# Kernel tuning notes

Hardware: AMD Instinct MI355X
Metric: run time of the kernel (lower is better)

## Reference

```python
import jax, jax.numpy as jnp
import numpy as np

K = 16  # top-k patches kept (module default)

def setup_inputs() -> dict:
    key = jax.random.key(0)
    ks = jax.random.split(key, 5)
    N, D, A, H = 100000, 1024, 128, 256
    x = jax.random.normal(ks[0], (N, D), dtype=jnp.float32)
    Wa1 = jax.random.normal(ks[1], (D, A), dtype=jnp.float32) * (1.0 / np.sqrt(D))
    ba1 = jnp.zeros((A,), dtype=jnp.float32)
    Wa2 = jax.random.normal(ks[2], (A, 1), dtype=jnp.float32) * (1.0 / np.sqrt(A))
    ba2 = jnp.zeros((1,), dtype=jnp.float32)
    Wc1 = jax.random.normal(ks[3], (D, H), dtype=jnp.float32) * (1.0 / np.sqrt(D))
    bc1 = jnp.zeros((H,), dtype=jnp.float32)
    Wc2 = jax.random.normal(ks[4], (H, 1), dtype=jnp.float32) * (1.0 / np.sqrt(H))
    bc2 = jnp.zeros((1,), dtype=jnp.float32)
    return {"x": x, "Wa1": Wa1, "ba1": ba1, "Wa2": Wa2, "ba2": ba2,
            "Wc1": Wc1, "bc1": bc1, "Wc2": Wc2, "bc2": bc2}

def reference(x, Wa1, ba1, Wa2, ba2, Wc1, bc1, Wc2, bc2):
    # attention logits: Linear -> tanh -> Linear, shape [N]
    scores = (jnp.tanh(x @ Wa1 + ba1) @ Wa2 + ba2)[:, 0]
    # top-k selection over patch dim (k < N here)
    top_vals, top_idx = jax.lax.top_k(scores, K)       # [K], [K]
    x_k = x[top_idx]                                    # [K, D] gather
    attn_w = jax.nn.softmax(top_vals)                   # renormalise over k
    slide_embedding = attn_w @ x_k                      # [D] weighted sum
    # classifier MLP (dropout is identity in eval)
    h = jax.nn.relu(slide_embedding @ Wc1 + bc1)
    logit = (h @ Wc2 + bc2)[0]
    # scatter attention weights back into full-length vector
    full_weights = jnp.zeros(x.shape[0], dtype=x.dtype).at[top_idx].set(attn_w)
    return logit, slide_embedding, full_weights, top_idx
```

## Files before the change

### kernel.cpp

```cpp
#include <hip/hip_runtime.h>
#include <cstddef>
#include <cstdint>

#define N_PATCH 100000
#define D_IN    1024
#define A_DIM   128
#define H_DIM   256
#define KTOP    16

#define OUT_LOGIT 0
#define OUT_EMB   1
#define OUT_FW    (1 + D_IN)
#define OUT_TOPI  (OUT_FW + N_PATCH)

#define WS_SCORES 0
#define WS_CANDV  (N_PATCH)
#define WS_CANDI  (N_PATCH + 4096)
#define WS_TOPI   (N_PATCH + 2 * 4096)
#define WS_EMB    (WS_TOPI + 16)
#define WS_HPART  (WS_EMB + D_IN)
#define WS_HP2    (WS_HPART + 16 * H_DIM)
#define WS_WPK    (WS_HP2 + 16 * KTOP * 128)

#define NB2A  256
#define CHUNK 391

typedef __attribute__((ext_vector_type(8))) short bf8_t;
typedef __attribute__((ext_vector_type(4))) float f4_t;

__global__ __launch_bounds__(256) void k_prepack(
    const float* __restrict__ Wa1, uint4* __restrict__ wpk)
{
    int t = blockIdx.x * 256 + threadIdx.x;
    int lane = t & 63;
    int nt   = (t >> 6) & 7;
    int ks   = t >> 9;
    int n  = nt * 16 + (lane & 15);
    int k0 = ks * 32 + ((lane >> 4) * 8);
    union { ushort u[8]; uint4 v; } o;
    #pragma unroll
    for (int j = 0; j < 8; ++j) {
        uint b = __float_as_uint(Wa1[(size_t)(k0 + j) * A_DIM + n]);
        o.u[j] = (ushort)((b + 0x7fffu + ((b >> 16) & 1u)) >> 16);
    }
    wpk[t] = o.v;
}

__device__ __forceinline__ void cvt8(const float4& a, const float4& b, bf8_t& out)
{
    union { uint u[4]; bf8_t v; } O;
    asm("v_cvt_pk_bf16_f32 %0, %1, %2" : "=v"(O.u[0]) : "v"(a.x), "v"(a.y));
    asm("v_cvt_pk_bf16_f32 %0, %1, %2" : "=v"(O.u[1]) : "v"(a.z), "v"(a.w));
    asm("v_cvt_pk_bf16_f32 %0, %1, %2" : "=v"(O.u[2]) : "v"(b.x), "v"(b.y));
    asm("v_cvt_pk_bf16_f32 %0, %1, %2" : "=v"(O.u[3]) : "v"(b.z), "v"(b.w));
    out = O.v;
}

#define MFMA_BF16 __builtin_amdgcn_mfma_f32_16x16x32_bf16

#define BAR_LDS() do {                                          \
    asm volatile("s_waitcnt lgkmcnt(0)" ::: "memory");          \
    __builtin_amdgcn_s_barrier();                               \
    asm volatile("" ::: "memory");                              \
} while (0)

#define LOADA(BUF, IT, PAR) do {                                               \
    const int kg = (((t0 + (IT)) & 15) * 2 + (PAR)) * 32;                      \
    A##BUF[0] = *(const float4*)(pa0 + kg);                                    \
    A##BUF[1] = *(const float4*)(pa0 + kg + 4);                                \
    A##BUF[2] = *(const float4*)(pa1 + kg);                                    \
    A##BUF[3] = *(const float4*)(pa1 + kg + 4);                                \
} while (0)

#define SCORE_STEP(IT, PAR, BUF, BUFP) do {                                    \
    bf8_t ah0, ah1;                                                            \
    cvt8(A##BUF[0], A##BUF[1], ah0);                                           \
    cvt8(A##BUF[2], A##BUF[3], ah1);                                           \
    if ((PAR) == 0) {                                                          \
        _Pragma("unroll")                                                      \
        for (int i = 0; i < 4; ++i) sB[(BUFP) ^ 1][tid + i * 256] = bpre[i];   \
        const int vtp = (t0 + (IT) + 2) & 15;                                  \
        _Pragma("unroll")                                                      \
        for (int i = 0; i < 4; ++i) bpre[i] = wpk[vtp * 1024 + tid + i * 256]; \
    }                                                                          \
    LOADA(BUF, (IT) + 2, PAR);                                                 \
    const bf8_t* sBf = (const bf8_t*)sB[BUFP] + (PAR) * 512;                   \
    _Pragma("unroll")                                                          \
    for (int nt = 0; nt < 8; nt += 2) {                                        \
        bf8_t b0 = sBf[nt * 64 + ln];                                          \
        bf8_t b1 = sBf[(nt + 1) * 64 + ln];                                    \
        acc[0][nt]     = MFMA_BF16(ah0, b0, acc[0][nt],     0, 0, 0);          \
        acc[1][nt]     = MFMA_BF16(ah1, b0, acc[1][nt],     0, 0, 0);          \
        acc[0][nt + 1] = MFMA_BF16(ah0, b1, acc[0][nt + 1], 0, 0, 0);          \
        acc[1][nt + 1] = MFMA_BF16(ah1, b1, acc[1][nt + 1], 0, 0, 0);          \
    }                                                                          \
    if (PAR) BAR_LDS();                                                        \
} while (0)

__global__ __launch_bounds__(256) void k_scores(
    const float* __restrict__ x, const uint4* __restrict__ wpk,
    const float* __restrict__ ba1, const float* __restrict__ Wa2,
    const float* __restrict__ ba2, float* __restrict__ scores)
{
    __shared__ uint4 sB[2][1024];

    const int tid = threadIdx.x;
    const int ln  = tid & 63;
    const int q   = ln >> 4;
    const int c   = ln & 15;
    const int wv  = tid >> 6;
    const int row0 = blockIdx.x * 128 + wv * 32;
    const int t0   = blockIdx.x & 15;

    const int r0 = min(row0 + c,      N_PATCH - 1);
    const int r1 = min(row0 + 16 + c, N_PATCH - 1);
    const float* pa0 = x + (size_t)r0 * D_IN + q * 8;
    const float* pa1 = x + (size_t)r1 * D_IN + q * 8;

    f4_t acc[2][8];
    #pragma unroll
    for (int rt = 0; rt < 2; ++rt)
        #pragma unroll
        for (int nt = 0; nt < 8; ++nt)
            acc[rt][nt] = (f4_t){0.f, 0.f, 0.f, 0.f};

    uint4 bpre[4];
    {
        uint4 b0[4];
        #pragma unroll
        for (int i = 0; i < 4; ++i) b0[i] = wpk[t0 * 1024 + tid + i * 256];
        #pragma unroll
        for (int i = 0; i < 4; ++i) sB[0][tid + i * 256] = b0[i];
    }
    {
        const int t1 = (t0 + 1) & 15;
        #pragma unroll
        for (int i = 0; i < 4; ++i) bpre[i] = wpk[t1 * 1024 + tid + i * 256];
    }

    float4 AE0[4], AE1[4], AO0[4], AO1[4];
    LOADA(E0, 0, 0);
    LOADA(E1, 0, 1);
    LOADA(O0, 1, 0);
    LOADA(O1, 1, 1);

    BAR_LDS();

    for (int it = 0; it < 16; it += 2) {
        SCORE_STEP(it,     0, E0, 0);
        SCORE_STEP(it,     1, E1, 0);
        SCORE_STEP(it + 1, 0, O0, 1);
        SCORE_STEP(it + 1, 1, O1, 1);
    }

    float b1v[8], w2v[8];
    #pragma unroll
    for (int nt = 0; nt < 8; ++nt) {
        b1v[nt] = ba1[nt * 16 + c];
        w2v[nt] = Wa2[nt * 16 + c];
    }
    const float b2 = ba2[0];

    #pragma unroll
    for (int rt = 0; rt < 2; ++rt)
        #pragma unroll
        for (int reg = 0; reg < 4; ++reg) {
            float p = 0.f;
            #pragma unroll
            for (int nt = 0; nt < 8; ++nt)
                p += tanhf(acc[rt][nt][reg] + b1v[nt]) * w2v[nt];
            #pragma unroll
            for (int off = 1; off < 16; off <<= 1)
                p += __shfl_xor(p, off, 64);
            if (c == 0) {
                int row = row0 + rt * 16 + q * 4 + reg;
                if (row < N_PATCH) scores[row] = p + b2;
            }
        }
}

__global__ __launch_bounds__(256) void k_topk_local(
    const float* __restrict__ scores, float* __restrict__ candv,
    int* __restrict__ candi, float* __restrict__ out_fw)
{
    __shared__ float sv[512];
    __shared__ float rv[256];
    __shared__ int   rs[256];
    const int tid  = threadIdx.x;
    const int base = blockIdx.x * CHUNK;

    for (int i = tid; i < 512; i += 256) {
        int g = base + i;
        sv[i] = (i < CHUNK && g < N_PATCH) ? scores[g] : -1e30f;
    }
    for (int i = tid; i < CHUNK; i += 256) {
        int g = base + i;
        if (g < N_PATCH) out_fw[g] = 0.f;
    }
    __syncthreads();

    for (int r = 0; r < KTOP; ++r) {
        float v1 = sv[tid], v2 = sv[tid + 256];
        float bv; int bs;
        if (v2 > v1) { bv = v2; bs = tid + 256; } else { bv = v1; bs = tid; }
        rv[tid] = bv; rs[tid] = bs;
        __syncthreads();
        for (int off = 128; off > 0; off >>= 1) {
            if (tid < off) {
                float ov = rv[tid + off]; int os = rs[tid + off];
                if (ov > rv[tid] || (ov == rv[tid] && os < rs[tid])) {
                    rv[tid] = ov; rs[tid] = os;
                }
            }
            __syncthreads();
        }
        if (tid == 0) {
            int s = rs[0];
            candv[blockIdx.x * KTOP + r] = rv[0];
            candi[blockIdx.x * KTOP + r] = base + s;
            sv[s] = -1e30f;
        }
        __syncthreads();
    }
}

__global__ __launch_bounds__(256) void k_select(
    const float* __restrict__ candv, const int* __restrict__ candi,
    int* __restrict__ topi_ws)
{
    __shared__ float cv[4096];
    __shared__ int   ci[4096];
    __shared__ float rv[256];
    __shared__ int   rgx[256];
    __shared__ int   rsl[256];
    const int tid = threadIdx.x;

    for (int i = tid; i < 4096; i += 256) { cv[i] = candv[i]; ci[i] = candi[i]; }
    __syncthreads();

    for (int r = 0; r < KTOP; ++r) {
        float bv = -1e38f; int bg = 0x7fffffff; int bs = tid * 16;
        #pragma unroll
        for (int i = 0; i < 16; ++i) {
            int s = tid * 16 + i;
            float v = cv[s]; int g = ci[s];
            if (v > bv || (v == bv && g < bg)) { bv = v; bg = g; bs = s; }
        }
        rv[tid] = bv; rgx[tid] = bg; rsl[tid] = bs;
        __syncthreads();
        for (int off = 128; off > 0; off >>= 1) {
            if (tid < off) {
                if (rv[tid + off] > rv[tid] ||
                    (rv[tid + off] == rv[tid] && rgx[tid + off] < rgx[tid])) {
                    rv[tid] = rv[tid + off]; rgx[tid] = rgx[tid + off]; rsl[tid] = rsl[tid + off];
                }
            }
            __syncthreads();
        }
        if (tid == 0) {
            topi_ws[r] = rgx[0]; cv[rsl[0]] = -1e30f;
        }
        __syncthreads();
    }
}

__global__ __launch_bounds__(256) void k_rescore(
    const float* __restrict__ x, const float* __restrict__ Wa1,
    const int* __restrict__ topi_ws, float* __restrict__ hp)
{
    __shared__ float sx[KTOP][64];
    __shared__ int   sti[KTOP];
    const int b = blockIdx.x, tid = threadIdx.x;
    if (tid < KTOP) sti[tid] = topi_ws[tid];
    __syncthreads();
    for (int i = tid; i < KTOP * 64; i += 256) {
        int r = i >> 6, d = i & 63;
        sx[r][d] = x[(size_t)sti[r] * D_IN + b * 64 + d];
    }
    __syncthreads();

    const int n = tid & 127, h = tid >> 7;
    float ac[8];
    #pragma unroll
    for (int rr = 0; rr < 8; ++rr) ac[rr] = 0.f;
    #pragma unroll 4
    for (int d = 0; d < 64; ++d) {
        const float w = Wa1[(size_t)(b * 64 + d) * A_DIM + n];
        #pragma unroll
        for (int rr = 0; rr < 8; ++rr)
            ac[rr] = fmaf(sx[h * 8 + rr][d], w, ac[rr]);
    }
    #pragma unroll
    for (int rr = 0; rr < 8; ++rr)
        hp[((size_t)b * KTOP + h * 8 + rr) * 128 + n] = ac[rr];
}

__global__ __launch_bounds__(256) void k_final2(
    const float* __restrict__ hp, const float* __restrict__ ba1,
    const float* __restrict__ Wa2, const float* __restrict__ ba2,
    const float* __restrict__ x, const int* __restrict__ topi_ws,
    float* __restrict__ out, float* __restrict__ emb)
{
    __shared__ float sred[KTOP][128];
    __shared__ int   topi[KTOP];
    __shared__ float exv[KTOP];
    __shared__ float attn[KTOP];
    __shared__ int   order[KTOP];
    const int tid = threadIdx.x;
    if (tid < KTOP) topi[tid] = topi_ws[tid];

    {
        const int n = tid & 127, h = tid >> 7;
        const float bn = ba1[n], wn = Wa2[n];
        #pragma unroll
        for (int rr = 0; rr < 8; ++rr) {
            const int r = h * 8 + rr;
            float s = 0.f;
            #pragma unroll
            for (int b = 0; b < 16; ++b)
                s += hp[((size_t)b * KTOP + r) * 128 + n];
            sred[r][n] = tanhf(s + bn) * wn;
        }
    }
    __syncthreads();
    if (tid < KTOP) {
        float s = ba2[0];
        for (int n = 0; n < 128; ++n) s += sred[tid][n];
        exv[tid] = s;
    }
    __syncthreads();

    if (tid == 0) {
        #pragma unroll
        for (int k2 = 0; k2 < KTOP; ++k2) order[k2] = k2;
        for (int a2 = 1; a2 < KTOP; ++a2)
            for (int b2 = a2; b2 > 0; --b2) {
                int i1 = order[b2 - 1], i2 = order[b2];
                bool sw = (exv[i2] > exv[i1]) ||
                          (exv[i2] == exv[i1] && topi[i2] < topi[i1]);
                if (sw) { order[b2 - 1] = i2; order[b2] = i1; } else break;
            }
        float mx = exv[order[0]];
        float ssum = 0.f;
        for (int k2 = 0; k2 < KTOP; ++k2) {
            float e = expf(exv[order[k2]] - mx);
            attn[k2] = e; ssum += e;
        }
        float inv = 1.f / ssum;
        for (int k2 = 0; k2 < KTOP; ++k2) attn[k2] *= inv;
    }
    __syncthreads();

    if (tid < KTOP) {
        int src = order[tid];
        out[OUT_TOPI + tid] = (float)topi[src];
        out[OUT_FW + topi[src]] = attn[tid];
    }

    float4 e = {0.f, 0.f, 0.f, 0.f};
    #pragma unroll
    for (int k2 = 0; k2 < KTOP; ++k2) {
        const int src = order[k2];
        const float a = attn[k2];
        const float4 xv = *(const float4*)(x + (size_t)topi[src] * D_IN + tid * 4);
        e.x = fmaf(a, xv.x, e.x);
        e.y = fmaf(a, xv.y, e.y);
        e.z = fmaf(a, xv.z, e.z);
        e.w = fmaf(a, xv.w, e.w);
    }
    out[OUT_EMB + tid * 4 + 0] = e.x;
    out[OUT_EMB + tid * 4 + 1] = e.y;
    out[OUT_EMB + tid * 4 + 2] = e.z;
    out[OUT_EMB + tid * 4 + 3] = e.w;
    *(float4*)(emb + tid * 4) = e;
}

__global__ __launch_bounds__(256) void k_mlp1(
    const float* __restrict__ emb, const float* __restrict__ Wc1,
    float* __restrict__ hpart)
{
    __shared__ float se[64];
    const int b = blockIdx.x, tid = threadIdx.x;
    if (tid < 64) se[tid] = emb[b * 64 + tid];
    __syncthreads();
    float p = 0.f;
    #pragma unroll 8
    for (int d = 0; d < 64; ++d)
        p = fmaf(se[d], Wc1[(size_t)(b * 64 + d) * H_DIM + tid], p);
    hpart[b * H_DIM + tid] = p;
}

__global__ __launch_bounds__(256) void k_logit(
    const float* __restrict__ hpart, const float* __restrict__ bc1,
    const float* __restrict__ Wc2, const float* __restrict__ bc2,
    float* __restrict__ out)
{
    __shared__ float red[256];
    const int tid = threadIdx.x;
    float h = bc1[tid];
    #pragma unroll
    for (int i = 0; i < 16; ++i) h += hpart[i * H_DIM + tid];
    h = fmaxf(h, 0.f) * Wc2[tid];
    red[tid] = h;
    __syncthreads();
    for (int off = 128; off > 0; off >>= 1) {
        if (tid < off) red[tid] += red[tid + off];
        __syncthreads();
    }
    if (tid == 0) out[OUT_LOGIT] = red[0] + bc2[0];
}

extern "C" void kernel_launch(void* const* d_in, const int* in_sizes, int n_in,
                              void* d_out, int out_size, void* d_ws, size_t ws_size,
                              hipStream_t stream)
{
    const float* x   = (const float*)d_in[0];
    const float* Wa1 = (const float*)d_in[1];
    const float* ba1 = (const float*)d_in[2];
    const float* Wa2 = (const float*)d_in[3];
    const float* ba2 = (const float*)d_in[4];
    const float* Wc1 = (const float*)d_in[5];
    const float* bc1 = (const float*)d_in[6];
    const float* Wc2 = (const float*)d_in[7];
    const float* bc2 = (const float*)d_in[8];
    float* out = (float*)d_out;
    float* ws  = (float*)d_ws;

    float* scores = ws + WS_SCORES;
    float* candv  = ws + WS_CANDV;
    int*   candi  = (int*)(ws + WS_CANDI);
    int*   topi   = (int*)(ws + WS_TOPI);
    float* emb    = ws + WS_EMB;
    float* hpart  = ws + WS_HPART;
    float* hp2    = ws + WS_HP2;
    uint4* wpk    = (uint4*)(ws + WS_WPK);

    dim3 blk(256);
    k_prepack<<<64, blk, 0, stream>>>(Wa1, wpk);
    k_scores<<<(N_PATCH + 127) / 128, blk, 0, stream>>>(x, wpk, ba1, Wa2, ba2, scores);
    k_topk_local<<<NB2A, blk, 0, stream>>>(scores, candv, candi, out + OUT_FW);
    k_select<<<1, blk, 0, stream>>>(candv, candi, topi);
    k_rescore<<<16, blk, 0, stream>>>(x, Wa1, topi, hp2);
    k_final2<<<1, blk, 0, stream>>>(hp2, ba1, Wa2, ba2, x, topi, out, emb);
    k_mlp1<<<16, blk, 0, stream>>>(emb, Wc1, hpart);
    k_logit<<<1, blk, 0, stream>>>(hpart, bc1, Wc2, bc2, out);
}
```

Baseline: 704.3 us.

## Fuse per-block top-k into scoring kernel and merge tail stages into one kernel

Each scoring block now runs a wavefront-level top-16 over its 128 scores in LDS and writes candidates directly, so the full scores array and the separate local top-k kernel go away. Selection, fp32 rescoring of the winners, softmax, embedding and the first classifier layer are merged into one 16-block tail kernel. Every block redundantly repeats the 12.5k-candidate selection and the full 1024-deep rescore, so the tail does more work per block in exchange for fewer launches. Zeroing of the full weight vector moves into the prepack kernel.

After: 907.0 us. +28.8%, slower.

```diff
diff --git a/kernel.cpp b/kernel.cpp
--- a/kernel.cpp
+++ b/kernel.cpp
@@ -13,23 +13,20 @@
 #define OUT_FW    (1 + D_IN)
 #define OUT_TOPI  (OUT_FW + N_PATCH)
 
-#define WS_SCORES 0
-#define WS_CANDV  (N_PATCH)
-#define WS_CANDI  (N_PATCH + 4096)
-#define WS_TOPI   (N_PATCH + 2 * 4096)
-#define WS_EMB    (WS_TOPI + 16)
-#define WS_HPART  (WS_EMB + D_IN)
-#define WS_HP2    (WS_HPART + 16 * H_DIM)
-#define WS_WPK    (WS_HP2 + 16 * KTOP * 128)
-
-#define NB2A  256
-#define CHUNK 391
+#define NBLK   782
+#define NCAND  (NBLK * KTOP)
+
+#define WS_CANDV  0
+#define WS_CANDI  12544
+#define WS_HPART  25088
+#define WS_WPK    29184
 
 typedef __attribute__((ext_vector_type(8))) short bf8_t;
 typedef __attribute__((ext_vector_type(4))) float f4_t;
 
 __global__ __launch_bounds__(256) void k_prepack(
-    const float* __restrict__ Wa1, uint4* __restrict__ wpk)
+    const float* __restrict__ Wa1, uint4* __restrict__ wpk,
+    float* __restrict__ out_fw)
 {
     int t = blockIdx.x * 256 + threadIdx.x;
     int lane = t & 63;
@@ -44,6 +41,7 @@
         o.u[j] = (ushort)((b + 0x7fffu + ((b >> 16) & 1u)) >> 16);
     }
     wpk[t] = o.v;
+    for (int i = t; i < N_PATCH; i += 64 * 256) out_fw[i] = 0.f;
 }
 
 __device__ __forceinline__ void cvt8(const float4& a, const float4& b, bf8_t& out)
@@ -100,7 +98,8 @@
 __global__ __launch_bounds__(256) void k_scores(
     const float* __restrict__ x, const uint4* __restrict__ wpk,
     const float* __restrict__ ba1, const float* __restrict__ Wa2,
-    const float* __restrict__ ba2, float* __restrict__ scores)
+    const float* __restrict__ ba2, float* __restrict__ candv,
+    int* __restrict__ candi)
 {
     __shared__ uint4 sB[2][1024];
 
@@ -161,6 +160,7 @@
     }
     const float b2 = ba2[0];
 
+    float* sS = (float*)(void*)sB;
     #pragma unroll
     for (int rt = 0; rt < 2; ++rt)
         #pragma unroll
@@ -173,69 +173,73 @@
             for (int off = 1; off < 16; off <<= 1)
                 p += __shfl_xor(p, off, 64);
             if (c == 0) {
-                int row = row0 + rt * 16 + q * 4 + reg;
-                if (row < N_PATCH) scores[row] = p + b2;
-            }
-        }
-}
-
-__global__ __launch_bounds__(256) void k_topk_local(
-    const float* __restrict__ scores, float* __restrict__ candv,
-    int* __restrict__ candi, float* __restrict__ out_fw)
-{
-    __shared__ float sv[512];
-    __shared__ float rv[256];
-    __shared__ int   rs[256];
-    const int tid  = threadIdx.x;
-    const int base = blockIdx.x * CHUNK;
-
-    for (int i = tid; i < 512; i += 256) {
-        int g = base + i;
-        sv[i] = (i < CHUNK && g < N_PATCH) ? scores[g] : -1e30f;
-    }
-    for (int i = tid; i < CHUNK; i += 256) {
-        int g = base + i;
-        if (g < N_PATCH) out_fw[g] = 0.f;
-    }
-    __syncthreads();
-
-    for (int r = 0; r < KTOP; ++r) {
-        float v1 = sv[tid], v2 = sv[tid + 256];
-        float bv; int bs;
-        if (v2 > v1) { bv = v2; bs = tid + 256; } else { bv = v1; bs = tid; }
-        rv[tid] = bv; rs[tid] = bs;
-        __syncthreads();
-        for (int off = 128; off > 0; off >>= 1) {
-            if (tid < off) {
-                float ov = rv[tid + off]; int os = rs[tid + off];
-                if (ov > rv[tid] || (ov == rv[tid] && os < rs[tid])) {
-                    rv[tid] = ov; rs[tid] = os;
-                }
-            }
-            __syncthreads();
-        }
-        if (tid == 0) {
-            int s = rs[0];
-            candv[blockIdx.x * KTOP + r] = rv[0];
-            candi[blockIdx.x * KTOP + r] = base + s;
-            sv[s] = -1e30f;
-        }
-        __syncthreads();
-    }
-}
-
-__global__ __launch_bounds__(256) void k_select(
+                int lrow = rt * 16 + q * 4 + reg;
+                int row  = row0 + lrow;
+                sS[wv * 32 + lrow] = (row < N_PATCH) ? (p + b2) : -1e30f;
+            }
+        }
+    __syncthreads();
+
+    if (wv == 0) {
+        float v0 = sS[ln], v1 = sS[ln + 64];
+        int   i0 = ln,     i1 = ln + 64;
+        for (int r = 0; r < KTOP; ++r) {
+            bool f = (v0 > v1) || (v0 == v1 && i0 < i1);
+            float mv = f ? v0 : v1;
+            int   mi = f ? i0 : i1;
+            #pragma unroll
+            for (int off = 1; off < 64; off <<= 1) {
+                float ov = __shfl_xor(mv, off, 64);
+                int   oi = __shfl_xor(mi, off, 64);
+                if (ov > mv || (ov == mv && oi < mi)) { mv = ov; mi = oi; }
+            }
+            if (ln == 0) {
+                candv[blockIdx.x * KTOP + r] = mv;
+                candi[blockIdx.x * KTOP + r] = blockIdx.x * 128 + mi;
+            }
+            if (mi == i0) v0 = -1e30f;
+            if (mi == i1) v1 = -1e30f;
+        }
+    }
+}
+
+__global__ __launch_bounds__(256) void k_tail(
     const float* __restrict__ candv, const int* __restrict__ candi,
-    int* __restrict__ topi_ws)
-{
-    __shared__ float cv[4096];
-    __shared__ int   ci[4096];
+    const float* __restrict__ x, const float* __restrict__ Wa1,
+    const float* __restrict__ ba1, const float* __restrict__ Wa2,
+    const float* __restrict__ ba2, const float* __restrict__ Wc1,
+    float* __restrict__ out, float* __restrict__ hpart)
+{
+    __shared__ float svals[4096];
+    __shared__ int   sidx[4096];
     __shared__ float rv[256];
     __shared__ int   rgx[256];
     __shared__ int   rsl[256];
+    __shared__ int   sti[KTOP];
+    __shared__ float exv[KTOP];
+    __shared__ float attn[KTOP];
+    __shared__ int   order[KTOP];
+    __shared__ float semb[64];
     const int tid = threadIdx.x;
 
-    for (int i = tid; i < 4096; i += 256) { cv[i] = candv[i]; ci[i] = candi[i]; }
+    float tv[16]; int ti[16];
+    #pragma unroll
+    for (int j = 0; j < 16; ++j) { tv[j] = -1e30f; ti[j] = 0x7fffffff; }
+    for (int i = tid; i < NCAND; i += 256) {
+        float v = candv[i]; int gi = candi[i];
+        if (v > tv[15] || (v == tv[15] && gi < ti[15])) {
+            tv[15] = v; ti[15] = gi;
+            #pragma unroll
+            for (int j = 15; j > 0; --j) {
+                if (tv[j] > tv[j-1] || (tv[j] == tv[j-1] && ti[j] < ti[j-1])) {
+                    float fv = tv[j]; tv[j] = tv[j-1]; tv[j-1] = fv;
+                    int   fi = ti[j]; ti[j] = ti[j-1]; ti[j-1] = fi;
+                } else break;
+            }
+        }
+    }
+    #pragma unroll
+    for (int j = 0; j < 16; ++j) { svals[tid * 16 + j] = tv[j]; sidx[tid * 16 + j] = ti[j]; }
     __syncthreads();
 
     for (int r = 0; r < KTOP; ++r) {
@@ -243,7 +247,7 @@
         #pragma unroll
         for (int i = 0; i < 16; ++i) {
             int s = tid * 16 + i;
-            float v = cv[s]; int g = ci[s];
+            float v = svals[s]; int g = sidx[s];
             if (v > bv || (v == bv && g < bg)) { bv = v; bg = g; bs = s; }
         }
         rv[tid] = bv; rgx[tid] = bg; rsl[tid] = bs;
@@ -257,76 +261,34 @@
             }
             __syncthreads();
         }
-        if (tid == 0) {
-            topi_ws[r] = rgx[0]; cv[rsl[0]] = -1e30f;
-        }
+        if (tid == 0) { sti[r] = rgx[0]; svals[rsl[0]] = -1e30f; }
         __syncthreads();
     }
-}
-
-__global__ __launch_bounds__(256) void k_rescore(
-    const float* __restrict__ x, const float* __restrict__ Wa1,
-    const int* __restrict__ topi_ws, float* __restrict__ hp)
-{
-    __shared__ float sx[KTOP][64];
-    __shared__ int   sti[KTOP];
-    const int b = blockIdx.x, tid = threadIdx.x;
-    if (tid < KTOP) sti[tid] = topi_ws[tid];
-    __syncthreads();
-    for (int i = tid; i < KTOP * 64; i += 256) {
-        int r = i >> 6, d = i & 63;
-        sx[r][d] = x[(size_t)sti[r] * D_IN + b * 64 + d];
-    }
-    __syncthreads();
-
-    const int n = tid & 127, h = tid >> 7;
-    float ac[8];
-    #pragma unroll
-    for (int rr = 0; rr < 8; ++rr) ac[rr] = 0.f;
-    #pragma unroll 4
-    for (int d = 0; d < 64; ++d) {
-        const float w = Wa1[(size_t)(b * 64 + d) * A_DIM + n];
-        #pragma unroll
-        for (int rr = 0; rr < 8; ++rr)
-            ac[rr] = fmaf(sx[h * 8 + rr][d], w, ac[rr]);
-    }
-    #pragma unroll
-    for (int rr = 0; rr < 8; ++rr)
-        hp[((size_t)b * KTOP + h * 8 + rr) * 128 + n] = ac[rr];
-}
-
-__global__ __launch_bounds__(256) void k_final2(
-    const float* __restrict__ hp, const float* __restrict__ ba1,
-    const float* __restrict__ Wa2, const float* __restrict__ ba2,
-    const float* __restrict__ x, const int* __restrict__ topi_ws,
-    float* __restrict__ out, float* __restrict__ emb)
-{
-    __shared__ float sred[KTOP][128];
-    __shared__ int   topi[KTOP];
-    __shared__ float exv[KTOP];
-    __shared__ float attn[KTOP];
-    __shared__ int   order[KTOP];
-    const int tid = threadIdx.x;
-    if (tid < KTOP) topi[tid] = topi_ws[tid];
 
     {
-        const int n = tid & 127, h = tid >> 7;
-        const float bn = ba1[n], wn = Wa2[n];
-        #pragma unroll
-        for (int rr = 0; rr < 8; ++rr) {
-            const int r = h * 8 + rr;
-            float s = 0.f;
-            #pragma unroll
-            for (int b = 0; b < 16; ++b)
-                s += hp[((size_t)b * KTOP + r) * 128 + n];
-            sred[r][n] = tanhf(s + bn) * wn;
-        }
-    }
-    __syncthreads();
-    if (tid < KTOP) {
-        float s = ba2[0];
-        for (int n = 0; n < 128; ++n) s += sred[tid][n];
-        exv[tid] = s;
+        const int row = tid >> 4, cc = tid & 15, n0 = cc * 8;
+        const float* xr = x + (size_t)sti[row] * D_IN;
+        float ac[8];
+        #pragma unroll
+        for (int j = 0; j < 8; ++j) ac[j] = 0.f;
+        #pragma unroll 4
+        for (int d = 0; d < D_IN; ++d) {
+            const float xv = xr[d];
+            const float4 w0 = *(const float4*)(Wa1 + (size_t)d * A_DIM + n0);
+            const float4 w1 = *(const float4*)(Wa1 + (size_t)d * A_DIM + n0 + 4);
+            ac[0] = fmaf(xv, w0.x, ac[0]); ac[1] = fmaf(xv, w0.y, ac[1]);
+            ac[2] = fmaf(xv, w0.z, ac[2]); ac[3] = fmaf(xv, w0.w, ac[3]);
+            ac[4] = fmaf(xv, w1.x, ac[4]); ac[5] = fmaf(xv, w1.y, ac[5]);
+            ac[6] = fmaf(xv, w1.z, ac[6]); ac[7] = fmaf(xv, w1.w, ac[7]);
+        }
+        float p = 0.f;
+        #pragma unroll
+        for (int j = 0; j < 8; ++j)
+            p += tanhf(ac[j] + ba1[n0 + j]) * Wa2[n0 + j];
+        #pragma unroll
+        for (int off = 1; off < 16; off <<= 1)
+            p += __shfl_xor(p, off, 64);
+        if (cc == 0) exv[row] = p + ba2[0];
     }
     __syncthreads();
 
@@ -337,7 +299,7 @@
             for (int b2 = a2; b2 > 0; --b2) {
                 int i1 = order[b2 - 1], i2 = order[b2];
                 bool sw = (exv[i2] > exv[i1]) ||
-                          (exv[i2] == exv[i1] && topi[i2] < topi[i1]);
+                          (exv[i2] == exv[i1] && sti[i2] < sti[i1]);
                 if (sw) { order[b2 - 1] = i2; order[b2] = i1; } else break;
             }
         float mx = exv[order[0]];
@@ -351,43 +313,31 @@
     }
     __syncthreads();
 
-    if (tid < KTOP) {
+    if (blockIdx.x == 0 && tid < KTOP) {
         int src = order[tid];
-        out[OUT_TOPI + tid] = (float)topi[src];
-        out[OUT_FW + topi[src]] = attn[tid];
-    }
-
-    float4 e = {0.f, 0.f, 0.f, 0.f};
-    #pragma unroll
-    for (int k2 = 0; k2 < KTOP; ++k2) {
-        const int src = order[k2];
-        const float a = attn[k2];
-        const float4 xv = *(const float4*)(x + (size_t)topi[src] * D_IN + tid * 4);
-        e.x = fmaf(a, xv.x, e.x);
-        e.y = fmaf(a, xv.y, e.y);
-        e.z = fmaf(a, xv.z, e.z);
-        e.w = fmaf(a, xv.w, e.w);
-    }
-    out[OUT_EMB + tid * 4 + 0] = e.x;
-    out[OUT_EMB + tid * 4 + 1] = e.y;
-    out[OUT_EMB + tid * 4 + 2] = e.z;
-    out[OUT_EMB + tid * 4 + 3] = e.w;
-    *(float4*)(emb + tid * 4) = e;
-}
-
-__global__ __launch_bounds__(256) void k_mlp1(
-    const float* __restrict__ emb, const float* __restrict__ Wc1,
-    float* __restrict__ hpart)
-{
-    __shared__ float se[64];
-    const int b = blockIdx.x, tid = threadIdx.x;
-    if (tid < 64) se[tid] = emb[b * 64 + tid];
-    __syncthreads();
-    float p = 0.f;
-    #pragma unroll 8
-    for (int d = 0; d < 64; ++d)
-        p = fmaf(se[d], Wc1[(size_t)(b * 64 + d) * H_DIM + tid], p);
-    hpart[b * H_DIM + tid] = p;
+        out[OUT_TOPI + tid] = (float)sti[src];
+        out[OUT_FW + sti[src]] = attn[tid];
+    }
+
+    if (tid < 64) {
+        const int d = blockIdx.x * 64 + tid;
+        float e = 0.f;
+        #pragma unroll
+        for (int k2 = 0; k2 < KTOP; ++k2)
+            e = fmaf(attn[k2], x[(size_t)sti[order[k2]] * D_IN + d], e);
+        out[OUT_EMB + d] = e;
+        semb[tid] = e;
+    }
+    __syncthreads();
+
+    {
+        float p = 0.f;
+        const float* wc = Wc1 + (size_t)blockIdx.x * 64 * H_DIM + tid;
+        #pragma unroll 8
+        for (int j = 0; j < 64; ++j)
+            p = fmaf(semb[j], wc[(size_t)j * H_DIM], p);
+        hpart[blockIdx.x * H_DIM + tid] = p;
+    }
 }
 
 __global__ __launch_bounds__(256) void k_logit(
@@ -426,22 +376,14 @@
     float* out = (float*)d_out;
     float* ws  = (float*)d_ws;
 
-    float* scores = ws + WS_SCORES;
-    float* candv  = ws + WS_CANDV;
-    int*   candi  = (int*)(ws + WS_CANDI);
-    int*   topi   = (int*)(ws + WS_TOPI);
-    float* emb    = ws + WS_EMB;
-    float* hpart  = ws + WS_HPART;
-    float* hp2    = ws + WS_HP2;
-    uint4* wpk    = (uint4*)(ws + WS_WPK);
+    float* candv = ws + WS_CANDV;
+    int*   candi = (int*)(ws + WS_CANDI);
+    float* hpart = ws + WS_HPART;
+    uint4* wpk   = (uint4*)(ws + WS_WPK);
 
     dim3 blk(256);
-    k_prepack<<<64, blk, 0, stream>>>(Wa1, wpk);
-    k_scores<<<(N_PATCH + 127) / 128, blk, 0, stream>>>(x, wpk, ba1, Wa2, ba2, scores);
-    k_topk_local<<<NB2A, blk, 0, stream>>>(scores, candv, candi, out + OUT_FW);
-    k_select<<<1, blk, 0, stream>>>(candv, candi, topi);
-    k_rescore<<<16, blk, 0, stream>>>(x, Wa1, topi, hp2);
-    k_final2<<<1, blk, 0, stream>>>(hp2, ba1, Wa2, ba2, x, topi, out, emb);
-    k_mlp1<<<16, blk, 0, stream>>>(emb, Wc1, hpart);
+    k_prepack<<<64, blk, 0, stream>>>(Wa1, wpk, out + OUT_FW);
+    k_scores<<<NBLK, blk, 0, stream>>>(x, wpk, ba1, Wa2, ba2, candv, candi);
+    k_tail<<<16, blk, 0, stream>>>(candv, candi, x, Wa1, ba1, Wa2, ba2, Wc1, out, hpart);
     k_logit<<<1, blk, 0, stream>>>(hpart, bc1, Wc2, bc2, out);
 }
```
